# Performance work log

Hardware: AMD Instinct MI355X
Metric: run time of the kernel (lower is better)

The kernel has to match this reference:

```python
import jax, jax.numpy as jnp
import numpy as np

N_HEAD = 12
N_EMBD = 768

def setup_inputs() -> dict:
    key = jax.random.key(0)
    ks = jax.random.split(key, 5)
    B, T, C = 4, 2048, N_EMBD
    x = jax.random.normal(ks[0], (B, T, C), dtype=jnp.float32)
    # c_attn: Linear(C, 3C); c_proj: Linear(C, C). Torch Linear stores W as [out,in].
    w_attn = jax.random.normal(ks[1], (3 * C, C), dtype=jnp.float32) * (1.0 / np.sqrt(C))
    b_attn = jnp.zeros((3 * C,), dtype=jnp.float32)
    w_proj = jax.random.normal(ks[2], (C, C), dtype=jnp.float32) * (1.0 / np.sqrt(C))
    b_proj = jnp.zeros((C,), dtype=jnp.float32)
    return {"x": x, "w_attn": w_attn, "b_attn": b_attn, "w_proj": w_proj, "b_proj": b_proj}

def reference(x, w_attn, b_attn, w_proj, b_proj):
    B, T, C = x.shape
    H = N_HEAD
    hs = C // H
    qkv = jnp.einsum('btc,oc->bto', x, w_attn) + b_attn  # [B,T,3C]
    q, k, v = jnp.split(qkv, 3, axis=-1)
    # [B,T,C] -> [B,H,T,hs]
    q = q.reshape(B, T, H, hs).transpose(0, 2, 1, 3)
    k = k.reshape(B, T, H, hs).transpose(0, 2, 1, 3)
    v = v.reshape(B, T, H, hs).transpose(0, 2, 1, 3)
    scale = 1.0 / np.sqrt(hs)
    att = jnp.einsum('bhqd,bhkd->bhqk', q, k) * scale  # [B,H,T,T]
    causal = jnp.tril(jnp.ones((T, T), dtype=bool))
    att = jnp.where(causal[None, None], att, -jnp.inf)
    att = jax.nn.softmax(att, axis=-1)
    y = jnp.einsum('bhqk,bhkd->bhqd', att, v)  # [B,H,T,hs]
    y = y.transpose(0, 2, 1, 3).reshape(B, T, C)
    return jnp.einsum('btc,oc->bto', y, w_proj) + b_proj
```

## Files before the change

kernel.cpp:

```cpp
#include <hip/hip_runtime.h>
#include <hip/hip_bf16.h>


typedef __attribute__((ext_vector_type(8))) short bf16x8;
typedef __attribute__((ext_vector_type(4))) short bf16x4;
typedef __attribute__((ext_vector_type(4))) float f32x4;

#define MFMA16(a, b, c) __builtin_amdgcn_mfma_f32_16x16x32_bf16((a), (b), (c), 0, 0, 0)

__device__ __forceinline__ unsigned short f2bfbits(float f) {
  return __builtin_bit_cast(unsigned short, __float2bfloat16(f));
}
__device__ __forceinline__ float bf2f(short b) {
  return __uint_as_float(((unsigned)(unsigned short)b) << 16);
}
__device__ __forceinline__ float fast_exp2(float x) {
#if __has_builtin(__builtin_amdgcn_exp2f)
  return __builtin_amdgcn_exp2f(x);
#else
  return __expf(x * 0.6931471805599453f);
#endif
}
__device__ __forceinline__ float fmax3(float a, float b, float c) {
  return fmaxf(fmaxf(a, b), c);
}
__device__ __forceinline__ unsigned pk2bf(float lo, float hi) {
  return (__builtin_bit_cast(unsigned, hi) & 0xffff0000u) |
         (__builtin_bit_cast(unsigned, lo) >> 16);
}

__device__ __forceinline__ void gload_lds16(const void* g, void* l) {
  __builtin_amdgcn_global_load_lds((const __attribute__((address_space(1))) void*)g,
                                   (__attribute__((address_space(3))) void*)l, 16, 0, 0);
}

__global__ __launch_bounds__(256) void cvt3(const float* __restrict__ x,
                                            const float* __restrict__ wa,
                                            const float* __restrict__ wp,
                                            unsigned short* __restrict__ xb,
                                            unsigned short* __restrict__ wab,
                                            unsigned short* __restrict__ wpb) {
  int i = blockIdx.x * 256 + threadIdx.x;
  const float* in;
  unsigned short* out;
  int j;
  if (i < 1572864) { in = x; out = xb; j = i; }
  else if (i < 2015232) { in = wa; out = wab; j = i - 1572864; }
  else { in = wp; out = wpb; j = i - 2015232; }
  float4 f = ((const float4*)in)[j];
  bf16x4 o;
  o[0] = (short)f2bfbits(f.x); o[1] = (short)f2bfbits(f.y);
  o[2] = (short)f2bfbits(f.z); o[3] = (short)f2bfbits(f.w);
  ((bf16x4*)out)[j] = o;
}

template <typename OutT>
__global__ __launch_bounds__(256) void gemm_bt(const unsigned short* __restrict__ A,
                                               const unsigned short* __restrict__ Bt,
                                               const float* __restrict__ bias,
                                               OutT* __restrict__ C, int M, int N, int K) {
  __shared__ unsigned short As[128 * 64];
  __shared__ unsigned short Bs[128 * 64];
  const int tid = threadIdx.x;
  const int w = tid >> 6, l = tid & 63;
  const int g = l >> 4, li = l & 15;
  const int wm = w >> 1, wn = w & 1;
  const int m0 = blockIdx.y * 128, n0 = blockIdx.x * 128;

  const int scw = (l & 7) ^ ((l >> 3) & 7);
  const int swr = li & 7;

  f32x4 acc[4][4] = {};

  for (int kt = 0; kt < K; kt += 64) {
#pragma unroll
    for (int n = 0; n < 4; ++n) {
      int R = w * 32 + n * 8 + (l >> 3);
      gload_lds16(A + (long)(m0 + R) * K + kt + scw * 8, &As[(w * 32 + n * 8) * 64]);
      gload_lds16(Bt + (long)(n0 + R) * K + kt + scw * 8, &Bs[(w * 32 + n * 8) * 64]);
    }
    __syncthreads();
#pragma unroll
    for (int kk = 0; kk < 2; ++kk) {
      bf16x8 a[4], b[4];
#pragma unroll
      for (int m = 0; m < 4; ++m)
        a[m] = *(const bf16x8*)&As[(wm * 64 + m * 16 + li) * 64 + ((kk * 4 + g) ^ swr) * 8];
#pragma unroll
      for (int n = 0; n < 4; ++n)
        b[n] = *(const bf16x8*)&Bs[(wn * 64 + n * 16 + li) * 64 + ((kk * 4 + g) ^ swr) * 8];
#pragma unroll
      for (int m = 0; m < 4; ++m)
#pragma unroll
        for (int n = 0; n < 4; ++n) acc[m][n] = MFMA16(a[m], b[n], acc[m][n]);
    }
    __syncthreads();
  }

#pragma unroll
  for (int m = 0; m < 4; ++m) {
    int row = m0 + wm * 64 + m * 16 + 4 * g;
#pragma unroll
    for (int n = 0; n < 4; ++n) {
      int col = n0 + wn * 64 + n * 16 + li;
      float bi = bias[col];
#pragma unroll
      for (int r = 0; r < 4; ++r) {
        float v = acc[m][n][r] + bi;
        if constexpr (sizeof(OutT) == 2)
          C[(long)(row + r) * N + col] = (OutT)f2bfbits(v);
        else
          C[(long)(row + r) * N + col] = v;
      }
    }
  }
}

__global__ __launch_bounds__(64) void transpose_v(const unsigned short* __restrict__ qkv,
                                                  unsigned short* __restrict__ vt) {
  const int kt = blockIdx.x & 31, bh = blockIdx.x >> 5;
  const int b = bh / 12, h = bh - b * 12;
  const int l = threadIdx.x;
  const int ct = l & 7, cd = l >> 3;

  bf16x8 tin[8], tout[8];
#pragma unroll
  for (int i = 0; i < 8; ++i)
    tin[i] = *(const bf16x8*)(qkv + (long)(b * 2048 + kt * 64 + ct * 8 + i) * 2304 +
                              1536 + h * 64 + cd * 8);
#pragma unroll
  for (int j = 0; j < 8; ++j) {
#pragma unroll
    for (int i = 0; i < 8; ++i) tout[j][i] = tin[i][j];
    *(bf16x8*)(vt + (long)(bh * 64 + cd * 8 + j) * 2048 + kt * 64 + ct * 8) = tout[j];
  }
}

__device__ __forceinline__ bf16x8 scale_bf8(bf16x8 v, float c) {
  bf16x8 o;
#pragma unroll
  for (int j = 0; j < 8; ++j) o[j] = (short)f2bfbits(bf2f(v[j]) * c);
  return o;
}

__device__ __forceinline__ void softmax_state(f32x4* s, bool diag, int g, int li, int qloc,
                                              unsigned short* PsW, float& m, f32x4* o,
                                              f32x4& o4) {
  if (diag) {
#pragma unroll
    for (int kn = 0; kn < 4; ++kn)
#pragma unroll
      for (int r = 0; r < 4; ++r)
        if (kn * 16 + 4 * g + r > qloc) s[kn][r] = -1e30f;
  }
  float a = fmax3(s[0][0], s[0][1], s[0][2]);
  float b = fmax3(s[0][3], s[1][0], s[1][1]);
  float c = fmax3(s[1][2], s[1][3], s[2][0]);
  float d = fmax3(s[2][1], s[2][2], s[2][3]);
  float e = fmax3(s[3][0], s[3][1], s[3][2]);
  float pm = fmaxf(fmax3(a, b, c), fmax3(d, e, s[3][3]));
  pm = fmaxf(pm, __shfl_xor(pm, 16));
  pm = fmaxf(pm, __shfl_xor(pm, 32));

  if (!__all(pm - m <= 10.0f)) {
    float mn = fmaxf(m, pm);
    float alpha = fast_exp2(m - mn);
    m = mn;
    float alo[4];
#pragma unroll
    for (int r = 0; r < 4; ++r) alo[r] = __shfl(alpha, 20 * g + r);
#pragma unroll
    for (int dn = 0; dn < 4; ++dn)
#pragma unroll
      for (int r = 0; r < 4; ++r) o[dn][r] *= alo[r];
#pragma unroll
    for (int r = 0; r < 4; ++r) o4[r] *= alo[r];
  }

  const int swp = li & 7;
#pragma unroll
  for (int kn = 0; kn < 4; ++kn) {
    float e0 = fast_exp2(s[kn][0] - m);
    float e1 = fast_exp2(s[kn][1] - m);
    float e2 = fast_exp2(s[kn][2] - m);
    float e3 = fast_exp2(s[kn][3] - m);
    uint2 pk = {pk2bf(e0, e1), pk2bf(e2, e3)};
    *(uint2*)&PsW[li * 64 + ((kn * 2 + (g >> 1)) ^ swp) * 8 + (g & 1) * 4] = pk;
  }
}

template <bool DUAL>
__device__ __forceinline__ void attn_tile(const unsigned short* Ks, const unsigned short* Vs,
                                          unsigned short* PsH, unsigned short* PsL,
                                          const bf16x8* bqh, const bf16x8* bql,
                                          bool diagh, bool diagl, int g, int li, int qloc,
                                          float& mh, f32x4* oh, f32x4& oh4,
                                          float& ml, f32x4* ol, f32x4& ol4) {
  f32x4 sh[4], sl[4];
  __builtin_amdgcn_s_setprio(1);
#pragma unroll
  for (int kn = 0; kn < 4; ++kn) {
    int rr = kn * 16 + li, sw = rr & 7;
    f32x4 ah = {}, al = {};
#pragma unroll
    for (int kk = 0; kk < 2; ++kk) {
      bf16x8 ak = *(const bf16x8*)&Ks[rr * 64 + ((kk * 4 + g) ^ sw) * 8];
      ah = MFMA16(ak, bqh[kk], ah);
      if constexpr (DUAL) al = MFMA16(ak, bql[kk], al);
    }
    sh[kn] = ah;
    if constexpr (DUAL) sl[kn] = al;
  }
  __builtin_amdgcn_s_setprio(0);

  softmax_state(sh, diagh, g, li, qloc, PsH, mh, oh, oh4);
  if constexpr (DUAL) softmax_state(sl, diagl, g, li, qloc, PsL, ml, ol, ol4);

  bf16x8 vones;
#pragma unroll
  for (int j = 0; j < 8; ++j) vones[j] = (short)0x3F80;

  const int swp = li & 7;
  __builtin_amdgcn_s_setprio(1);
#pragma unroll
  for (int kk = 0; kk < 2; ++kk) {
    bf16x8 pah = *(const bf16x8*)&PsH[li * 64 + ((kk * 4 + g) ^ swp) * 8];
    bf16x8 pal;
    if constexpr (DUAL) pal = *(const bf16x8*)&PsL[li * 64 + ((kk * 4 + g) ^ swp) * 8];
#pragma unroll
    for (int dn = 0; dn < 4; ++dn) {
      int rv = dn * 16 + li;
      bf16x8 vb = *(const bf16x8*)&Vs[rv * 64 + ((kk * 4 + g) ^ (rv & 7)) * 8];
      oh[dn] = MFMA16(pah, vb, oh[dn]);
      if constexpr (DUAL) ol[dn] = MFMA16(pal, vb, ol[dn]);
    }
    oh4 = MFMA16(pah, vones, oh4);
    if constexpr (DUAL) ol4 = MFMA16(pal, vones, ol4);
  }
  __builtin_amdgcn_s_setprio(0);
}

__global__ __launch_bounds__(256, 3) void attn_fwd(const unsigned short* __restrict__ qkv,
                                                   const unsigned short* __restrict__ vt,
                                                   unsigned short* __restrict__ y) {
  const int orig = (blockIdx.x & 7) * 96 + (blockIdx.x >> 3);
  const int bh = orig >> 4, p = orig & 15;
  const int b = bh / 12, h = bh - b * 12;
  const int qlo = p, qhi = 31 - p;
  const int tid = threadIdx.x;
  const int w = tid >> 6, l = tid & 63;
  const int g = l >> 4, li = l & 15;
  const int qloc = w * 16 + li;

  __shared__ unsigned short Ks[2][64 * 64];
  __shared__ unsigned short Vs[2][64 * 64];
  __shared__ unsigned short Ps[8][16 * 64];
  unsigned short* PsH = &Ps[w][0];
  unsigned short* PsL = &Ps[4 + w][0];

  const unsigned short* base = qkv + (long)b * 2048 * 2304;

  const float QS = 0.18033688011112042f;
  bf16x8 bqlo[2], bqhi[2];
  {
    const unsigned short* qr = base + (long)(qlo * 64 + qloc) * 2304 + h * 64;
    bqlo[0] = scale_bf8(*(const bf16x8*)(qr + 8 * g), QS);
    bqlo[1] = scale_bf8(*(const bf16x8*)(qr + 32 + 8 * g), QS);
    qr = base + (long)(qhi * 64 + qloc) * 2304 + h * 64;
    bqhi[0] = scale_bf8(*(const bf16x8*)(qr + 8 * g), QS);
    bqhi[1] = scale_bf8(*(const bf16x8*)(qr + 32 + 8 * g), QS);
  }

  float m_lo = -1e30f, m_hi = -1e30f;
  f32x4 o_lo[4] = {}, o_hi[4] = {};
  f32x4 o4_lo = {}, o4_hi = {};

  const int sR = w * 8 + (l >> 3);
  const int sc = l & 7;

  int buf = 0;
  {
#pragma unroll
    for (int n = 0; n < 2; ++n) {
      int R = n * 32 + sR;
      int c = sc ^ (R & 7);
      gload_lds16(base + (long)R * 2304 + 768 + h * 64 + c * 8, &Ks[0][(n * 32 + w * 8) * 64]);
      gload_lds16(vt + (long)(bh * 64 + R) * 2048 + c * 8, &Vs[0][(n * 32 + w * 8) * 64]);
    }
  }
  __syncthreads();

  for (int kt = 0; kt <= qhi; ++kt) {
    if (kt < qhi) {
#pragma unroll
      for (int n = 0; n < 2; ++n) {
        int R = n * 32 + sR;
        int c = sc ^ (R & 7);
        gload_lds16(base + (long)((kt + 1) * 64 + R) * 2304 + 768 + h * 64 + c * 8,
                    &Ks[buf ^ 1][(n * 32 + w * 8) * 64]);
        gload_lds16(vt + (long)(bh * 64 + R) * 2048 + (kt + 1) * 64 + c * 8,
                    &Vs[buf ^ 1][(n * 32 + w * 8) * 64]);
      }
    }
    if (kt <= qlo)
      attn_tile<true>(Ks[buf], Vs[buf], PsH, PsL, bqhi, bqlo, kt == qhi, kt == qlo,
                      g, li, qloc, m_hi, o_hi, o4_hi, m_lo, o_lo, o4_lo);
    else
      attn_tile<false>(Ks[buf], Vs[buf], PsH, PsL, bqhi, bqlo, kt == qhi, false,
                       g, li, qloc, m_hi, o_hi, o4_hi, m_lo, o_lo, o4_lo);
    __syncthreads();
    buf ^= 1;
  }

#pragma unroll
  for (int t = 0; t < 2; ++t) {
    const f32x4* o = t ? o_hi : o_lo;
    const f32x4& o4 = t ? o4_hi : o4_lo;
    int qt = t ? qhi : qlo;
#pragma unroll
    for (int r = 0; r < 4; ++r) {
      float inv = 1.0f / o4[r];
      long row = (long)b * 2048 + qt * 64 + w * 16 + 4 * g + r;
#pragma unroll
      for (int dn = 0; dn < 4; ++dn)
        y[row * 768 + h * 64 + dn * 16 + li] = (unsigned short)f2bfbits(o[dn][r] * inv);
    }
  }
}

extern "C" void kernel_launch(void* const* d_in, const int* in_sizes, int n_in,
                              void* d_out, int out_size, void* d_ws, size_t ws_size,
                              hipStream_t stream) {
  const float* x      = (const float*)d_in[0];
  const float* w_attn = (const float*)d_in[1];
  const float* b_attn = (const float*)d_in[2];
  const float* w_proj = (const float*)d_in[3];
  const float* b_proj = (const float*)d_in[4];
  float* out = (float*)d_out;

  unsigned short* xb   = (unsigned short*)d_ws;
  unsigned short* wab  = xb + 6291456;
  unsigned short* wpb  = wab + 1769472;
  unsigned short* qkvb = wpb + 589824;
  unsigned short* yb   = qkvb + (long)8192 * 2304;
  unsigned short* vtb  = yb + 6291456;

  cvt3<<<8448, 256, 0, stream>>>(x, w_attn, w_proj, xb, wab, wpb);

  gemm_bt<unsigned short><<<dim3(18, 64), 256, 0, stream>>>(xb, wab, b_attn, qkvb, 8192, 2304, 768);
  transpose_v<<<1536, 64, 0, stream>>>(qkvb, vtb);
  attn_fwd<<<768, 256, 0, stream>>>(qkvb, vtb, yb);
  gemm_bt<float><<<dim3(6, 64), 256, 0, stream>>>(yb, wpb, b_proj, out, 8192, 768, 768);
}
```

Before: 140.5 us.

## Rewrite attention inner loop with 32x32 MFMA and register-resident P

```diff
diff --git a/kernel.cpp b/kernel.cpp
--- a/kernel.cpp
+++ b/kernel.cpp
@@ -5,8 +5,10 @@
 typedef __attribute__((ext_vector_type(8))) short bf16x8;
 typedef __attribute__((ext_vector_type(4))) short bf16x4;
 typedef __attribute__((ext_vector_type(4))) float f32x4;
+typedef __attribute__((ext_vector_type(16))) float f32x16;
 
 #define MFMA16(a, b, c) __builtin_amdgcn_mfma_f32_16x16x32_bf16((a), (b), (c), 0, 0, 0)
+#define MFMA32(a, b, c) __builtin_amdgcn_mfma_f32_32x32x16_bf16((a), (b), (c), 0, 0, 0)
 
 __device__ __forceinline__ unsigned short f2bfbits(float f) {
   return __builtin_bit_cast(unsigned short, __float2bfloat16(f));
@@ -20,9 +22,6 @@
 #else
   return __expf(x * 0.6931471805599453f);
 #endif
-}
-__device__ __forceinline__ float fmax3(float a, float b, float c) {
-  return fmaxf(fmaxf(a, b), c);
 }
 __device__ __forceinline__ unsigned pk2bf(float lo, float hi) {
   return (__builtin_bit_cast(unsigned, hi) & 0xffff0000u) |
@@ -143,104 +142,116 @@
   return o;
 }
 
-__device__ __forceinline__ void softmax_state(f32x4* s, bool diag, int g, int li, int qloc,
-                                              unsigned short* PsW, float& m, f32x4* o,
-                                              f32x4& o4) {
+__device__ __forceinline__ void softmax_pack32(f32x16& s0, f32x16& s1, bool diag, int hi,
+                                               int qloc, float& m, float& lsum, f32x16* o,
+                                               bf16x8* pa) {
   if (diag) {
 #pragma unroll
-    for (int kn = 0; kn < 4; ++kn)
-#pragma unroll
-      for (int r = 0; r < 4; ++r)
-        if (kn * 16 + 4 * g + r > qloc) s[kn][r] = -1e30f;
-  }
-  float a = fmax3(s[0][0], s[0][1], s[0][2]);
-  float b = fmax3(s[0][3], s[1][0], s[1][1]);
-  float c = fmax3(s[1][2], s[1][3], s[2][0]);
-  float d = fmax3(s[2][1], s[2][2], s[2][3]);
-  float e = fmax3(s[3][0], s[3][1], s[3][2]);
-  float pm = fmaxf(fmax3(a, b, c), fmax3(d, e, s[3][3]));
-  pm = fmaxf(pm, __shfl_xor(pm, 16));
+    for (int r = 0; r < 16; ++r) {
+      int cr = (r & 3) + 8 * (r >> 2) + 4 * hi;
+      if (cr > qloc) s0[r] = -1e30f;
+      if (32 + cr > qloc) s1[r] = -1e30f;
+    }
+  }
+  float pm = fmaxf(s0[0], s1[0]);
+#pragma unroll
+  for (int r = 1; r < 16; ++r) pm = fmaxf(pm, fmaxf(s0[r], s1[r]));
   pm = fmaxf(pm, __shfl_xor(pm, 32));
 
   if (!__all(pm - m <= 10.0f)) {
     float mn = fmaxf(m, pm);
     float alpha = fast_exp2(m - mn);
     m = mn;
-    float alo[4];
-#pragma unroll
-    for (int r = 0; r < 4; ++r) alo[r] = __shfl(alpha, 20 * g + r);
-#pragma unroll
-    for (int dn = 0; dn < 4; ++dn)
-#pragma unroll
-      for (int r = 0; r < 4; ++r) o[dn][r] *= alo[r];
-#pragma unroll
-    for (int r = 0; r < 4; ++r) o4[r] *= alo[r];
-  }
-
-  const int swp = li & 7;
-#pragma unroll
-  for (int kn = 0; kn < 4; ++kn) {
-    float e0 = fast_exp2(s[kn][0] - m);
-    float e1 = fast_exp2(s[kn][1] - m);
-    float e2 = fast_exp2(s[kn][2] - m);
-    float e3 = fast_exp2(s[kn][3] - m);
-    uint2 pk = {pk2bf(e0, e1), pk2bf(e2, e3)};
-    *(uint2*)&PsW[li * 64 + ((kn * 2 + (g >> 1)) ^ swp) * 8 + (g & 1) * 4] = pk;
+    lsum *= alpha;
+    float alo[16];
+#pragma unroll
+    for (int r = 0; r < 16; ++r) alo[r] = __shfl(alpha, (r & 3) + 8 * (r >> 2) + 4 * hi);
+#pragma unroll
+    for (int dn = 0; dn < 2; ++dn)
+#pragma unroll
+      for (int r = 0; r < 16; ++r) o[dn][r] *= alo[r];
+  }
+
+  float ps = 0.f;
+  unsigned C0[8], C1[8];
+#pragma unroll
+  for (int mm = 0; mm < 4; ++mm) {
+    float e0 = fast_exp2(s0[4 * mm + 0] - m), e1 = fast_exp2(s0[4 * mm + 1] - m);
+    float e2 = fast_exp2(s0[4 * mm + 2] - m), e3 = fast_exp2(s0[4 * mm + 3] - m);
+    ps += (e0 + e1) + (e2 + e3);
+    C0[2 * mm] = pk2bf(e0, e1);
+    C0[2 * mm + 1] = pk2bf(e2, e3);
+    float f0 = fast_exp2(s1[4 * mm + 0] - m), f1 = fast_exp2(s1[4 * mm + 1] - m);
+    float f2 = fast_exp2(s1[4 * mm + 2] - m), f3 = fast_exp2(s1[4 * mm + 3] - m);
+    ps += (f0 + f1) + (f2 + f3);
+    C1[2 * mm] = pk2bf(f0, f1);
+    C1[2 * mm + 1] = pk2bf(f2, f3);
+  }
+  ps += __shfl_xor(ps, 32);
+  lsum += ps;
+
+#pragma unroll
+  for (int kn = 0; kn < 2; ++kn) {
+#pragma unroll
+    for (int k2 = 0; k2 < 2; ++k2) {
+      unsigned a0 = kn ? C1[4 * k2 + 0] : C0[4 * k2 + 0];
+      unsigned a1 = kn ? C1[4 * k2 + 1] : C0[4 * k2 + 1];
+      unsigned b0 = kn ? C1[4 * k2 + 2] : C0[4 * k2 + 2];
+      unsigned b1 = kn ? C1[4 * k2 + 3] : C0[4 * k2 + 3];
+      unsigned sa0 = (unsigned)__shfl_xor((int)a0, 32);
+      unsigned sa1 = (unsigned)__shfl_xor((int)a1, 32);
+      unsigned sb0 = (unsigned)__shfl_xor((int)b0, 32);
+      unsigned sb1 = (unsigned)__shfl_xor((int)b1, 32);
+      uint4 uu;
+      uu.x = hi ? sb0 : a0;
+      uu.y = hi ? sb1 : a1;
+      uu.z = hi ? b0 : sa0;
+      uu.w = hi ? b1 : sa1;
+      pa[kn * 2 + k2] = __builtin_bit_cast(bf16x8, uu);
+    }
   }
 }
 
 template <bool DUAL>
-__device__ __forceinline__ void attn_tile(const unsigned short* Ks, const unsigned short* Vs,
-                                          unsigned short* PsH, unsigned short* PsL,
-                                          const bf16x8* bqh, const bf16x8* bql,
-                                          bool diagh, bool diagl, int g, int li, int qloc,
-                                          float& mh, f32x4* oh, f32x4& oh4,
-                                          float& ml, f32x4* ol, f32x4& ol4) {
-  f32x4 sh[4], sl[4];
+__device__ __forceinline__ void attn_tile32(const unsigned short* Ks, const unsigned short* Vs,
+                                            const bf16x8* bqh, const bf16x8* bql,
+                                            bool diagh, bool diagl, int hi, int q31, int qloc,
+                                            float& mh, float& lh, f32x16* oh,
+                                            float& ml, float& ll, f32x16* ol) {
+  const int swz = q31 & 7;
+  f32x16 sh0 = {}, sh1 = {}, sl0 = {}, sl1 = {};
   __builtin_amdgcn_s_setprio(1);
 #pragma unroll
-  for (int kn = 0; kn < 4; ++kn) {
-    int rr = kn * 16 + li, sw = rr & 7;
-    f32x4 ah = {}, al = {};
-#pragma unroll
-    for (int kk = 0; kk < 2; ++kk) {
-      bf16x8 ak = *(const bf16x8*)&Ks[rr * 64 + ((kk * 4 + g) ^ sw) * 8];
-      ah = MFMA16(ak, bqh[kk], ah);
-      if constexpr (DUAL) al = MFMA16(ak, bql[kk], al);
-    }
-    sh[kn] = ah;
-    if constexpr (DUAL) sl[kn] = al;
+  for (int dk = 0; dk < 4; ++dk) {
+    bf16x8 ak0 = *(const bf16x8*)&Ks[q31 * 64 + ((2 * dk + hi) ^ swz) * 8];
+    bf16x8 ak1 = *(const bf16x8*)&Ks[(32 + q31) * 64 + ((2 * dk + hi) ^ swz) * 8];
+    sh0 = MFMA32(ak0, bqh[dk], sh0);
+    sh1 = MFMA32(ak1, bqh[dk], sh1);
+    if constexpr (DUAL) {
+      sl0 = MFMA32(ak0, bql[dk], sl0);
+      sl1 = MFMA32(ak1, bql[dk], sl1);
+    }
   }
   __builtin_amdgcn_s_setprio(0);
 
-  softmax_state(sh, diagh, g, li, qloc, PsH, mh, oh, oh4);
-  if constexpr (DUAL) softmax_state(sl, diagl, g, li, qloc, PsL, ml, ol, ol4);
-
-  bf16x8 vones;
-#pragma unroll
-  for (int j = 0; j < 8; ++j) vones[j] = (short)0x3F80;
-
-  const int swp = li & 7;
+  bf16x8 paH[4], paL[4];
+  softmax_pack32(sh0, sh1, diagh, hi, qloc, mh, lh, oh, paH);
+  if constexpr (DUAL) softmax_pack32(sl0, sl1, diagl, hi, qloc, ml, ll, ol, paL);
+
   __builtin_amdgcn_s_setprio(1);
 #pragma unroll
-  for (int kk = 0; kk < 2; ++kk) {
-    bf16x8 pah = *(const bf16x8*)&PsH[li * 64 + ((kk * 4 + g) ^ swp) * 8];
-    bf16x8 pal;
-    if constexpr (DUAL) pal = *(const bf16x8*)&PsL[li * 64 + ((kk * 4 + g) ^ swp) * 8];
-#pragma unroll
-    for (int dn = 0; dn < 4; ++dn) {
-      int rv = dn * 16 + li;
-      bf16x8 vb = *(const bf16x8*)&Vs[rv * 64 + ((kk * 4 + g) ^ (rv & 7)) * 8];
-      oh[dn] = MFMA16(pah, vb, oh[dn]);
-      if constexpr (DUAL) ol[dn] = MFMA16(pal, vb, ol[dn]);
-    }
-    oh4 = MFMA16(pah, vones, oh4);
-    if constexpr (DUAL) ol4 = MFMA16(pal, vones, ol4);
+  for (int ks = 0; ks < 4; ++ks) {
+#pragma unroll
+    for (int dn = 0; dn < 2; ++dn) {
+      bf16x8 vb = *(const bf16x8*)&Vs[(dn * 32 + q31) * 64 + ((2 * ks + hi) ^ swz) * 8];
+      oh[dn] = MFMA32(paH[ks], vb, oh[dn]);
+      if constexpr (DUAL) ol[dn] = MFMA32(paL[ks], vb, ol[dn]);
+    }
   }
   __builtin_amdgcn_s_setprio(0);
 }
 
-__global__ __launch_bounds__(256, 3) void attn_fwd(const unsigned short* __restrict__ qkv,
+__global__ __launch_bounds__(128, 2) void attn_fwd(const unsigned short* __restrict__ qkv,
                                                    const unsigned short* __restrict__ vt,
                                                    unsigned short* __restrict__ y) {
   const int orig = (blockIdx.x & 7) * 96 + (blockIdx.x >> 3);
@@ -249,43 +260,38 @@
   const int qlo = p, qhi = 31 - p;
   const int tid = threadIdx.x;
   const int w = tid >> 6, l = tid & 63;
-  const int g = l >> 4, li = l & 15;
-  const int qloc = w * 16 + li;
+  const int q31 = l & 31, hi = l >> 5;
+  const int qloc = w * 32 + q31;
 
   __shared__ unsigned short Ks[2][64 * 64];
   __shared__ unsigned short Vs[2][64 * 64];
-  __shared__ unsigned short Ps[8][16 * 64];
-  unsigned short* PsH = &Ps[w][0];
-  unsigned short* PsL = &Ps[4 + w][0];
 
   const unsigned short* base = qkv + (long)b * 2048 * 2304;
 
   const float QS = 0.18033688011112042f;
-  bf16x8 bqlo[2], bqhi[2];
+  bf16x8 bqhi[4], bqlo[4];
   {
-    const unsigned short* qr = base + (long)(qlo * 64 + qloc) * 2304 + h * 64;
-    bqlo[0] = scale_bf8(*(const bf16x8*)(qr + 8 * g), QS);
-    bqlo[1] = scale_bf8(*(const bf16x8*)(qr + 32 + 8 * g), QS);
-    qr = base + (long)(qhi * 64 + qloc) * 2304 + h * 64;
-    bqhi[0] = scale_bf8(*(const bf16x8*)(qr + 8 * g), QS);
-    bqhi[1] = scale_bf8(*(const bf16x8*)(qr + 32 + 8 * g), QS);
-  }
-
-  float m_lo = -1e30f, m_hi = -1e30f;
-  f32x4 o_lo[4] = {}, o_hi[4] = {};
-  f32x4 o4_lo = {}, o4_hi = {};
-
-  const int sR = w * 8 + (l >> 3);
-  const int sc = l & 7;
+    const unsigned short* qr = base + (long)(qhi * 64 + qloc) * 2304 + h * 64 + 8 * hi;
+#pragma unroll
+    for (int dk = 0; dk < 4; ++dk) bqhi[dk] = scale_bf8(*(const bf16x8*)(qr + dk * 16), QS);
+    qr = base + (long)(qlo * 64 + qloc) * 2304 + h * 64 + 8 * hi;
+#pragma unroll
+    for (int dk = 0; dk < 4; ++dk) bqlo[dk] = scale_bf8(*(const bf16x8*)(qr + dk * 16), QS);
+  }
+
+  float m_lo = -1e30f, l_lo = 0.f, m_hi = -1e30f, l_hi = 0.f;
+  f32x16 o_lo[2] = {}, o_hi[2] = {};
+
+  const int sR8 = l >> 3, sc = l & 7;
 
   int buf = 0;
   {
 #pragma unroll
-    for (int n = 0; n < 2; ++n) {
-      int R = n * 32 + sR;
+    for (int i = 0; i < 4; ++i) {
+      int R = w * 32 + i * 8 + sR8;
       int c = sc ^ (R & 7);
-      gload_lds16(base + (long)R * 2304 + 768 + h * 64 + c * 8, &Ks[0][(n * 32 + w * 8) * 64]);
-      gload_lds16(vt + (long)(bh * 64 + R) * 2048 + c * 8, &Vs[0][(n * 32 + w * 8) * 64]);
+      gload_lds16(base + (long)R * 2304 + 768 + h * 64 + c * 8, &Ks[0][(w * 32 + i * 8) * 64]);
+      gload_lds16(vt + (long)(bh * 64 + R) * 2048 + c * 8, &Vs[0][(w * 32 + i * 8) * 64]);
     }
   }
   __syncthreads();
@@ -293,37 +299,38 @@
   for (int kt = 0; kt <= qhi; ++kt) {
     if (kt < qhi) {
 #pragma unroll
-      for (int n = 0; n < 2; ++n) {
-        int R = n * 32 + sR;
+      for (int i = 0; i < 4; ++i) {
+        int R = w * 32 + i * 8 + sR8;
         int c = sc ^ (R & 7);
         gload_lds16(base + (long)((kt + 1) * 64 + R) * 2304 + 768 + h * 64 + c * 8,
-                    &Ks[buf ^ 1][(n * 32 + w * 8) * 64]);
+                    &Ks[buf ^ 1][(w * 32 + i * 8) * 64]);
         gload_lds16(vt + (long)(bh * 64 + R) * 2048 + (kt + 1) * 64 + c * 8,
-                    &Vs[buf ^ 1][(n * 32 + w * 8) * 64]);
+                    &Vs[buf ^ 1][(w * 32 + i * 8) * 64]);
       }
     }
     if (kt <= qlo)
-      attn_tile<true>(Ks[buf], Vs[buf], PsH, PsL, bqhi, bqlo, kt == qhi, kt == qlo,
-                      g, li, qloc, m_hi, o_hi, o4_hi, m_lo, o_lo, o4_lo);
+      attn_tile32<true>(Ks[buf], Vs[buf], bqhi, bqlo, kt == qhi, kt == qlo, hi, q31, qloc,
+                        m_hi, l_hi, o_hi, m_lo, l_lo, o_lo);
     else
-      attn_tile<false>(Ks[buf], Vs[buf], PsH, PsL, bqhi, bqlo, kt == qhi, false,
-                       g, li, qloc, m_hi, o_hi, o4_hi, m_lo, o_lo, o4_lo);
+      attn_tile32<false>(Ks[buf], Vs[buf], bqhi, bqlo, kt == qhi, false, hi, q31, qloc,
+                         m_hi, l_hi, o_hi, m_lo, l_lo, o_lo);
     __syncthreads();
     buf ^= 1;
   }
 
 #pragma unroll
   for (int t = 0; t < 2; ++t) {
-    const f32x4* o = t ? o_hi : o_lo;
-    const f32x4& o4 = t ? o4_hi : o4_lo;
+    const f32x16* o = t ? o_hi : o_lo;
+    float inv = 1.0f / (t ? l_hi : l_lo);
     int qt = t ? qhi : qlo;
 #pragma unroll
-    for (int r = 0; r < 4; ++r) {
-      float inv = 1.0f / o4[r];
-      long row = (long)b * 2048 + qt * 64 + w * 16 + 4 * g + r;
-#pragma unroll
-      for (int dn = 0; dn < 4; ++dn)
-        y[row * 768 + h * 64 + dn * 16 + li] = (unsigned short)f2bfbits(o[dn][r] * inv);
+    for (int r = 0; r < 16; ++r) {
+      int cr = (r & 3) + 8 * (r >> 2) + 4 * hi;
+      float iq = __shfl(inv, (r & 3) + 8 * (r >> 2) + 4 * hi);
+      long row = (long)b * 2048 + qt * 64 + w * 32 + cr;
+#pragma unroll
+      for (int dn = 0; dn < 2; ++dn)
+        y[row * 768 + h * 64 + dn * 32 + q31] = (unsigned short)f2bfbits(o[dn][r] * iq);
     }
   }
 }
@@ -349,6 +356,6 @@
 
   gemm_bt<unsigned short><<<dim3(18, 64), 256, 0, stream>>>(xb, wab, b_attn, qkvb, 8192, 2304, 768);
   transpose_v<<<1536, 64, 0, stream>>>(qkvb, vtb);
-  attn_fwd<<<768, 256, 0, stream>>>(qkvb, vtb, yb);
+  attn_fwd<<<768, 128, 0, stream>>>(qkvb, vtb, yb);
   gemm_bt<float><<<dim3(6, 64), 256, 0, stream>>>(yb, wpb, b_proj, out, 8192, 768, 768);
 }
```

Result: slower. 179.2 us (+27.5%).
